# Kernel optimization log

Measured on AMD Instinct MI355X. Metric: run time of the kernel, lower is better.

Reference implementation:

```python
import jax, jax.numpy as jnp
import numpy as np

B, T = 64, 500
NUM_CONCEPT, DIM, SIZE_MEM = 1024, 64, 50


def setup_inputs() -> dict:
    key = jax.random.key(0)
    ks = jax.random.split(key, 16)
    d = DIM

    def lin(k, fin, fout):
        k1, k2 = jax.random.split(k)
        s = 1.0 / np.sqrt(fin)
        return (jax.random.uniform(k1, (fin, fout), jnp.float32, -s, s),
                jax.random.uniform(k2, (fout,), jnp.float32, -s, s))

    Wf, bf = lin(ks[4], 2 * d, d)
    We, be = lin(ks[5], d, d)
    Wa, ba = lin(ks[6], d, d)
    Wab, bab = lin(ks[7], d, 1)
    Wd, bd = lin(ks[8], d, 1)
    return {
        'concept_seq': jax.random.randint(ks[0], (B, T), 0, NUM_CONCEPT),
        'correct_seq': jax.random.randint(ks[1], (B, T), 0, 2),
        'num_concept': NUM_CONCEPT,
        'embed_key': jax.random.normal(ks[2], (NUM_CONCEPT, d), jnp.float32),
        'embed_value': jax.random.normal(ks[3], (2 * NUM_CONCEPT, d), jnp.float32),
        'Mk': jax.random.normal(ks[9], (SIZE_MEM, d), jnp.float32) * np.sqrt(2.0 / d),
        'Mv0': jax.random.normal(ks[10], (SIZE_MEM, d), jnp.float32) * np.sqrt(2.0 / d),
        'Wf': Wf, 'bf': bf, 'We': We, 'be': be, 'Wa': Wa, 'ba': ba,
        'Wab': Wab, 'bab': bab, 'Wd': Wd, 'bd': bd,
    }


def _forward(concept_seq, correct_seq, num_concept, embed_key, embed_value,
             Mk, Mv0, Wf, bf, We, be, Wa, ba, Wab, bab, Wd, bd):
    x = concept_seq + num_concept * correct_seq          # [B,T]
    k = embed_key[concept_seq]                           # [B,T,d]
    v = embed_value[x]                                   # [B,T,d]
    w = jax.nn.softmax(jnp.einsum('btd,sd->bts', k, Mk), axis=-1)  # [B,T,S]
    e = jax.nn.sigmoid(v @ We + be)                      # [B,T,d]
    a = jnp.tanh(v @ Wa + ba)                            # [B,T,d]

    bsz = concept_seq.shape[0]
    Mv_init = jnp.broadcast_to(Mv0, (bsz,) + Mv0.shape)  # [B,S,d]

    def step(Mvt, inp):
        wt, et, at = inp                                 # [B,S],[B,d],[B,d]
        u = wt[:, :, None]
        Mv_new = Mvt * (1.0 - u * et[:, None, :]) + u * at[:, None, :]
        return Mv_new, Mvt                               # emit pre-update state

    wT = jnp.swapaxes(w, 0, 1)                           # [T,B,S]
    eT = jnp.swapaxes(e, 0, 1)
    aT = jnp.swapaxes(a, 0, 1)
    _, Mv_pre = jax.lax.scan(step, Mv_init, (wT, eT, aT))  # [T,B,S,d]

    r = jnp.einsum('tbs,tbsd->btd', wT, Mv_pre)          # read content [B,T,d]
    f = jnp.tanh(jnp.concatenate([r, k], axis=-1) @ Wf + bf)
    stu_ability = jnp.tanh(f @ Wab + bab)                # [B,T,1] (dropout = eval identity)
    que_diff = jnp.tanh(k @ Wd + bd)                     # [B,T,1]
    return jax.nn.sigmoid(3.0 * stu_ability - que_diff)[..., 0]  # [B,T]


def reference(concept_seq, correct_seq, num_concept, embed_key, embed_value,
              Mk, Mv0, Wf, bf, We, be, Wa, ba, Wab, bab, Wd, bd):
    return _forward(concept_seq, correct_seq, num_concept, embed_key, embed_value,
                    Mk, Mv0, Wf, bf, We, be, Wa, ba, Wab, bab, Wd, bd)
```

## Files before the change

kernel.cpp:

```cpp
#include <hip/hip_runtime.h>
#include <hip/hip_bf16.h>
#include <math.h>

#define BB 64
#define TT 500
#define DD 64
#define SS 50
#define CH 20
#define NCH (TT / CH)

typedef float v2f __attribute__((ext_vector_type(2)));

__device__ __forceinline__ float sigmoidf_(float x) { return 1.0f / (1.0f + __expf(-x)); }

#define PIN() asm volatile("" ::: "memory")

__global__ __launch_bounds__(64) void k1_tables(
    const float* __restrict__ embed_key,
    const float* __restrict__ embed_value,
    const float* __restrict__ Mk,
    const float* __restrict__ We, const float* __restrict__ be,
    const float* __restrict__ Wa, const float* __restrict__ ba,
    int ncon, int nv,
    float* __restrict__ wTab, float* __restrict__ eaTab)
{
    const int lane = threadIdx.x;
    if ((int)blockIdx.x < ncon) {
        const int c = blockIdx.x;
        __shared__ float mkS[SS][DD + 1];
        __shared__ float kS[DD];
        kS[lane] = embed_key[c * DD + lane];
        for (int s = 0; s < SS; ++s)
            mkS[s][lane] = Mk[s * DD + lane];
        __syncthreads();

        float sc = -1e30f;
        if (lane < SS) {
            float acc = 0.f;
            #pragma unroll
            for (int dd = 0; dd < DD; ++dd)
                acc = fmaf(kS[dd], mkS[lane][dd], acc);
            sc = acc;
        }
        float m = sc;
        #pragma unroll
        for (int off = 32; off >= 1; off >>= 1)
            m = fmaxf(m, __shfl_xor(m, off));
        float ex = (lane < SS) ? __expf(sc - m) : 0.f;
        float ssum = ex;
        #pragma unroll
        for (int off = 32; off >= 1; off >>= 1)
            ssum += __shfl_xor(ssum, off);
        if (lane < SS)
            wTab[c * SS + lane] = ex / ssum;
    } else {
        const int x = blockIdx.x - ncon;
        __shared__ float vS[DD];
        vS[lane] = embed_value[x * DD + lane];
        __syncthreads();
        float acc_e = be[lane];
        float acc_a = ba[lane];
        #pragma unroll
        for (int i = 0; i < DD; ++i) {
            const float vi = vS[i];
            acc_e = fmaf(vi, We[i * DD + lane], acc_e);
            acc_a = fmaf(vi, Wa[i * DD + lane], acc_a);
        }
        float2 ea;
        ea.x = sigmoidf_(acc_e);
        ea.y = tanhf(acc_a);
        *(float2*)&eaTab[((size_t)x * DD + lane) * 2] = ea;
    }
}

#define STAGE_ISSUE(T0) {                                                    \
    _Pragma("unroll")                                                        \
    for (int kk = 0; kk < 5; ++kk) {                                         \
        const int idx_ = lane + 64 * kk;                                     \
        const int tt_ = idx_ >> 4, j_ = idx_ & 15;                           \
        const int s_ = st + j_;                                              \
        wr[kk] = (s_ < en) ? wTab[cL[(T0) + tt_] * SS + s_] : 0.f;           \
    }                                                                        \
    _Pragma("unroll")                                                        \
    for (int tt = 0; tt < CH; ++tt) {                                        \
        const int xx_ = xL[(T0) + tt];                                       \
        ear[tt] = *(const float2*)&eaTab[((size_t)xx_ * DD + lane) * 2];     \
    } }

#define STAGE_WRITE(BUF) {                                                   \
    _Pragma("unroll")                                                        \
    for (int kk = 0; kk < 5; ++kk) {                                         \
        const int idx_ = lane + 64 * kk;                                     \
        wL[BUF][idx_ >> 4][idx_ & 15] = wr[kk];                              \
    }                                                                        \
    _Pragma("unroll")                                                        \
    for (int tt = 0; tt < CH; ++tt)                                          \
        eaL[BUF][tt][lane] = ear[tt];                                        \
    }

#define PKSTEP(W2, JJ) {                                                     \
    const v2f mv_ = Mv2[JJ];                                                 \
    r2 = __builtin_elementwise_fma(W2, mv_, r2);                             \
    const v2f g_ = __builtin_elementwise_fma(e2, mv_, na2);                  \
    Mv2[JJ] = __builtin_elementwise_fma(-(W2), g_, mv_); }

__global__ __launch_bounds__(64, 1) void k2_scan(
    const int* __restrict__ cseq,
    const int* __restrict__ corr,
    const int* __restrict__ ncp,
    const float* __restrict__ wTab,
    const float* __restrict__ eaTab,
    const float* __restrict__ Mv0,
    float* __restrict__ rPart)
{
    const int b = blockIdx.x >> 2;
    const int sgB = blockIdx.x & 3;
    const int lane = threadIdx.x;
    const int nc = ncp[0];

    __shared__ int xL[TT];
    __shared__ int cL[TT];
    __shared__ float __align__(16) wL[2][CH][16];
    __shared__ float2 __align__(8) eaL[2][CH][DD];

    for (int i = lane; i < TT; i += 64) {
        const int c = cseq[b * TT + i];
        cL[i] = c;
        xL[i] = c + nc * corr[b * TT + i];
    }
    __syncthreads();

    const int st = (SS * sgB) >> 2;
    const int en = (SS * (sgB + 1)) >> 2;

    v2f Mv2[7];
    #pragma unroll
    for (int jj = 0; jj < 7; ++jj) {
        const int s0 = st + 2 * jj, s1 = s0 + 1;
        v2f m;
        m.x = (s0 < en) ? Mv0[s0 * DD + lane] : 0.f;
        m.y = (s1 < en) ? Mv0[s1 * DD + lane] : 0.f;
        Mv2[jj] = m;
    }

    float* rp = rPart + ((size_t)sgB * BB + b) * TT * DD + lane;

    float wr[5];
    float2 ear[CH];

    STAGE_ISSUE(0)
    STAGE_WRITE(0)

    for (int ch = 0; ch < NCH; ++ch) {
        const int buf = ch & 1;
        if (ch + 1 < NCH) {
            STAGE_ISSUE((ch + 1) * CH)
            PIN();
        }
        const int T0 = ch * CH;
        #pragma unroll
        for (int tc = 0; tc < CH; ++tc) {
            const float4 wq0 = *(const float4*)&wL[buf][tc][0];
            const float4 wq1 = *(const float4*)&wL[buf][tc][4];
            const float4 wq2 = *(const float4*)&wL[buf][tc][8];
            const v2f   w6_ = *(const v2f*)  &wL[buf][tc][12];
            const float2 ea = eaL[buf][tc][lane];
            const v2f e2  = {ea.x, ea.x};
            const v2f na2 = {-ea.y, -ea.y};
            const v2f w0_ = {wq0.x, wq0.y};
            const v2f w1_ = {wq0.z, wq0.w};
            const v2f w2_ = {wq1.x, wq1.y};
            const v2f w3_ = {wq1.z, wq1.w};
            const v2f w4_ = {wq2.x, wq2.y};
            const v2f w5_ = {wq2.z, wq2.w};
            v2f r2 = {0.f, 0.f};
            PKSTEP(w0_, 0) PKSTEP(w1_, 1) PKSTEP(w2_, 2) PKSTEP(w3_, 3)
            PKSTEP(w4_, 4) PKSTEP(w5_, 5) PKSTEP(w6_, 6)
            rp[(size_t)(T0 + tc) * DD] = r2.x + r2.y;
        }
        if (ch + 1 < NCH)
            STAGE_WRITE((ch + 1) & 1)
    }
}

__global__ __launch_bounds__(256) void k3_output(
    const int* __restrict__ cseq,
    const float* __restrict__ embed_key,
    const float* __restrict__ rPart,
    const float* __restrict__ Wf, const float* __restrict__ bf,
    const float* __restrict__ Wab, const float* __restrict__ bab,
    const float* __restrict__ Wd, const float* __restrict__ bd,
    float* __restrict__ out)
{
    const int tid = threadIdx.x;
    const int tx = tid & 15, ty = tid >> 4;
    const int bt0 = blockIdx.x * 64;

    __shared__ float __align__(16) wfS[128][64];
    __shared__ float __align__(16) catT[128][68];
    __shared__ float qS[64];
    __shared__ float wdS[64];
    __shared__ float redS[64][17];

    #pragma unroll
    for (int k = 0; k < 8; ++k) {
        const int idx = tid + k * 256;
        ((float4*)wfS)[idx] = ((const float4*)Wf)[idx];
    }
    if (tid < 64) wdS[tid] = Wd[tid];

    {
        const int d = tid & 63;
        const int g = tid >> 6;
        #pragma unroll
        for (int m = 0; m < 16; ++m) {
            const int btl = g + 4 * m;
            const int bt = bt0 + btl;
            const int c = cseq[bt];
            const size_t o = (size_t)bt * DD + d;
            const float r = rPart[o]
                          + rPart[(size_t)1 * BB * TT * DD + o]
                          + rPart[(size_t)2 * BB * TT * DD + o]
                          + rPart[(size_t)3 * BB * TT * DD + o];
            catT[d][btl] = r;
            catT[64 + d][btl] = embed_key[c * DD + d];
        }
    }
    __syncthreads();

    if (tid < 64) {
        const int btl = tid;
        float q = 0.f;
        #pragma unroll
        for (int i = 0; i < DD; ++i)
            q = fmaf(catT[64 + i][btl], wdS[i], q);
        qS[btl] = q;
    }

    float acc[4][4] = {{0.f}};
    #pragma unroll 8
    for (int i = 0; i < 128; ++i) {
        const float4 wf = *(const float4*)&wfS[i][tx * 4];
        const float4 ct = *(const float4*)&catT[i][ty * 4];
        acc[0][0] = fmaf(ct.x, wf.x, acc[0][0]);
        acc[0][1] = fmaf(ct.x, wf.y, acc[0][1]);
        acc[0][2] = fmaf(ct.x, wf.z, acc[0][2]);
        acc[0][3] = fmaf(ct.x, wf.w, acc[0][3]);
        acc[1][0] = fmaf(ct.y, wf.x, acc[1][0]);
        acc[1][1] = fmaf(ct.y, wf.y, acc[1][1]);
        acc[1][2] = fmaf(ct.y, wf.z, acc[1][2]);
        acc[1][3] = fmaf(ct.y, wf.w, acc[1][3]);
        acc[2][0] = fmaf(ct.z, wf.x, acc[2][0]);
        acc[2][1] = fmaf(ct.z, wf.y, acc[2][1]);
        acc[2][2] = fmaf(ct.z, wf.z, acc[2][2]);
        acc[2][3] = fmaf(ct.z, wf.w, acc[2][3]);
        acc[3][0] = fmaf(ct.w, wf.x, acc[3][0]);
        acc[3][1] = fmaf(ct.w, wf.y, acc[3][1]);
        acc[3][2] = fmaf(ct.w, wf.z, acc[3][2]);
        acc[3][3] = fmaf(ct.w, wf.w, acc[3][3]);
    }

    #pragma unroll
    for (int ii = 0; ii < 4; ++ii) {
        float p = 0.f;
        #pragma unroll
        for (int jj = 0; jj < 4; ++jj) {
            const int j = tx * 4 + jj;
            const float f = tanhf(acc[ii][jj] + bf[j]);
            p = fmaf(f, Wab[j], p);
        }
        redS[ty * 4 + ii][tx] = p;
    }
    __syncthreads();

    if (tid < 64) {
        const int btl = tid;
        float s = 0.f;
        #pragma unroll
        for (int t2 = 0; t2 < 16; ++t2)
            s += redS[btl][t2];
        const float stu  = tanhf(s + bab[0]);
        const float diff = tanhf(qS[btl] + bd[0]);
        out[bt0 + btl] = sigmoidf_(3.0f * stu - diff);
    }
}

extern "C" void kernel_launch(void* const* d_in, const int* in_sizes, int n_in,
                              void* d_out, int out_size, void* d_ws, size_t ws_size,
                              hipStream_t stream)
{
    const int*   concept_seq = (const int*)  d_in[0];
    const int*   correct_seq = (const int*)  d_in[1];
    const int*   num_concept = (const int*)  d_in[2];
    const float* embed_key   = (const float*)d_in[3];
    const float* embed_value = (const float*)d_in[4];
    const float* Mk          = (const float*)d_in[5];
    const float* Mv0         = (const float*)d_in[6];
    const float* Wf          = (const float*)d_in[7];
    const float* bf          = (const float*)d_in[8];
    const float* We          = (const float*)d_in[9];
    const float* be          = (const float*)d_in[10];
    const float* Wa          = (const float*)d_in[11];
    const float* ba          = (const float*)d_in[12];
    const float* Wab         = (const float*)d_in[13];
    const float* bab         = (const float*)d_in[14];
    const float* Wd          = (const float*)d_in[15];
    const float* bd          = (const float*)d_in[16];
    float* out = (float*)d_out;

    const int NCON = in_sizes[3] / DD;
    const int NV   = in_sizes[4] / DD;

    float* wTab  = (float*)d_ws;
    float* eaTab = wTab + (size_t)NCON * SS;
    float* rPart = eaTab + (size_t)NV * DD * 2;

    k1_tables<<<NCON + NV, 64, 0, stream>>>(
        embed_key, embed_value, Mk, We, be, Wa, ba,
        NCON, NV, wTab, eaTab);

    k2_scan<<<BB * 4, 64, 0, stream>>>(
        concept_seq, correct_seq, num_concept,
        wTab, eaTab, Mv0, rPart);

    k3_output<<<(BB * TT) / 64, 256, 0, stream>>>(
        concept_seq, embed_key, rPart,
        Wf, bf, Wab, bab, Wd, bd, out);
}
```

Before: 170.7 us.

## Parallelize memory scan over time with chunked affine maps and replay

Replaces the sequential 500-step per-batch scan with a three-phase parallel scan. Each of 10 time chunks first computes its per-slot affine map (A, B). A combine kernel then chains those maps to get each chunk's starting memory state, and a replay kernel reruns every chunk from its start state to produce the read vectors. The four slot-group partial reads are also reduced in shared memory inside the replay kernel, so k3 reads a single r buffer instead of summing four partial buffers. This exposes far more blocks (640 vs 256) to the GPU at the cost of roughly doubling the scan arithmetic, adding two extra launches, and writing and reading extra A/B buffers.

```diff
diff --git a/kernel.cpp b/kernel.cpp
--- a/kernel.cpp
+++ b/kernel.cpp
@@ -6,14 +6,12 @@
 #define TT 500
 #define DD 64
 #define SS 50
-#define CH 20
-#define NCH (TT / CH)
+#define PP 10
+#define LL 50
 
 typedef float v2f __attribute__((ext_vector_type(2)));
 
 __device__ __forceinline__ float sigmoidf_(float x) { return 1.0f / (1.0f + __expf(-x)); }
-
-#define PIN() asm volatile("" ::: "memory")
 
 __global__ __launch_bounds__(64) void k1_tables(
     const float* __restrict__ embed_key,
@@ -73,120 +71,163 @@
     }
 }
 
-#define STAGE_ISSUE(T0) {                                                    \
-    _Pragma("unroll")                                                        \
-    for (int kk = 0; kk < 5; ++kk) {                                         \
-        const int idx_ = lane + 64 * kk;                                     \
-        const int tt_ = idx_ >> 4, j_ = idx_ & 15;                           \
-        const int s_ = st + j_;                                              \
-        wr[kk] = (s_ < en) ? wTab[cL[(T0) + tt_] * SS + s_] : 0.f;           \
-    }                                                                        \
-    _Pragma("unroll")                                                        \
-    for (int tt = 0; tt < CH; ++tt) {                                        \
-        const int xx_ = xL[(T0) + tt];                                       \
-        ear[tt] = *(const float2*)&eaTab[((size_t)xx_ * DD + lane) * 2];     \
-    } }
-
-#define STAGE_WRITE(BUF) {                                                   \
-    _Pragma("unroll")                                                        \
-    for (int kk = 0; kk < 5; ++kk) {                                         \
-        const int idx_ = lane + 64 * kk;                                     \
-        wL[BUF][idx_ >> 4][idx_ & 15] = wr[kk];                              \
-    }                                                                        \
-    _Pragma("unroll")                                                        \
-    for (int tt = 0; tt < CH; ++tt)                                          \
-        eaL[BUF][tt][lane] = ear[tt];                                        \
-    }
-
-#define PKSTEP(W2, JJ) {                                                     \
-    const v2f mv_ = Mv2[JJ];                                                 \
-    r2 = __builtin_elementwise_fma(W2, mv_, r2);                             \
-    const v2f g_ = __builtin_elementwise_fma(e2, mv_, na2);                  \
-    Mv2[JJ] = __builtin_elementwise_fma(-(W2), g_, mv_); }
-
-__global__ __launch_bounds__(64, 1) void k2_scan(
-    const int* __restrict__ cseq,
-    const int* __restrict__ corr,
+
+#define SCAN_STAGE()                                                          \
+    const int b = blockIdx.x / PP, p = blockIdx.x % PP;                       \
+    const int tid = threadIdx.x;                                              \
+    const int lane = tid & 63, sg = tid >> 6;                                 \
+    const int t0g = p * LL;                                                   \
+    if (tid < LL) {                                                           \
+        const int c = cseq[b * TT + t0g + tid];                               \
+        cL[tid] = c;                                                          \
+        xL[tid] = c + ncp[0] * corr[b * TT + t0g + tid];                      \
+    }                                                                         \
+    __syncthreads();                                                          \
+    for (int i = tid; i < LL * 64; i += 256) {                                \
+        const int t = i >> 6, l = i & 63;                                     \
+        const int sg_ = l >> 4, j_ = l & 15;                                  \
+        const int st_ = (SS * sg_) >> 2, en_ = (SS * (sg_ + 1)) >> 2;         \
+        const int s_ = st_ + j_;                                              \
+        wLds[t][l] = (s_ < en_) ? wTab[cL[t] * SS + s_] : 0.f;                \
+        eaLds[t][l] = *(const float2*)&eaTab[((size_t)xL[t] * DD + l) * 2];   \
+    }
+
+#define LOADW(t)                                                              \
+    const float4 wv0 = *(const float4*)&wLds[t][sg * 16];                     \
+    const float4 wv1 = *(const float4*)&wLds[t][sg * 16 + 4];                 \
+    const float4 wv2 = *(const float4*)&wLds[t][sg * 16 + 8];                 \
+    const v2f w6 = *(const v2f*)&wLds[t][sg * 16 + 12];                       \
+    const v2f w[7] = {{wv0.x, wv0.y}, {wv0.z, wv0.w}, {wv1.x, wv1.y},         \
+                      {wv1.z, wv1.w}, {wv2.x, wv2.y}, {wv2.z, wv2.w}, w6};
+
+__global__ __launch_bounds__(256) void k2a_maps(
+    const int* __restrict__ cseq, const int* __restrict__ corr,
     const int* __restrict__ ncp,
-    const float* __restrict__ wTab,
-    const float* __restrict__ eaTab,
+    const float* __restrict__ wTab, const float* __restrict__ eaTab,
+    float* __restrict__ Aout, float* __restrict__ Bout)
+{
+    __shared__ int cL[LL], xL[LL];
+    __shared__ float __align__(16) wLds[LL][64];
+    __shared__ float2 __align__(8) eaLds[LL][64];
+
+    SCAN_STAGE()
+    __syncthreads();
+
+    v2f A[7], Bc[7];
+    #pragma unroll
+    for (int j = 0; j < 7; ++j) { A[j] = (v2f){1.f, 1.f}; Bc[j] = (v2f){0.f, 0.f}; }
+
+    const v2f one2 = {1.f, 1.f};
+    #pragma unroll 2
+    for (int t = 0; t < LL; ++t) {
+        LOADW(t)
+        const float2 ea = eaLds[t][lane];
+        const v2f e2 = {ea.x, ea.x}, a2 = {ea.y, ea.y};
+        #pragma unroll
+        for (int j = 0; j < 7; ++j) {
+            const v2f al = __builtin_elementwise_fma(-w[j], e2, one2);
+            const v2f be = w[j] * a2;
+            A[j]  = al * A[j];
+            Bc[j] = __builtin_elementwise_fma(al, Bc[j], be);
+        }
+    }
+
+    const int st = (SS * sg) >> 2, en = (SS * (sg + 1)) >> 2;
+    float* Ap = Aout + (size_t)blockIdx.x * SS * DD;
+    float* Bp = Bout + (size_t)blockIdx.x * SS * DD;
+    #pragma unroll
+    for (int j = 0; j < 6; ++j) {
+        const int s0 = st + 2 * j;
+        Ap[(size_t)s0 * DD + lane] = A[j].x;
+        Ap[(size_t)(s0 + 1) * DD + lane] = A[j].y;
+        Bp[(size_t)s0 * DD + lane] = Bc[j].x;
+        Bp[(size_t)(s0 + 1) * DD + lane] = Bc[j].y;
+    }
+    if (st + 12 < en) {
+        Ap[(size_t)(st + 12) * DD + lane] = A[6].x;
+        Bp[(size_t)(st + 12) * DD + lane] = Bc[6].x;
+    }
+}
+
+__global__ __launch_bounds__(256) void k2b_combine(
     const float* __restrict__ Mv0,
-    float* __restrict__ rPart)
-{
-    const int b = blockIdx.x >> 2;
-    const int sgB = blockIdx.x & 3;
-    const int lane = threadIdx.x;
-    const int nc = ncp[0];
-
-    __shared__ int xL[TT];
-    __shared__ int cL[TT];
-    __shared__ float __align__(16) wL[2][CH][16];
-    __shared__ float2 __align__(8) eaL[2][CH][DD];
-
-    for (int i = lane; i < TT; i += 64) {
-        const int c = cseq[b * TT + i];
-        cL[i] = c;
-        xL[i] = c + nc * corr[b * TT + i];
+    float* __restrict__ Aio, const float* __restrict__ Bin)
+{
+    const int gid = blockIdx.x * 256 + threadIdx.x;
+    const int d = gid & 63;
+    const int s = (gid >> 6) % SS;
+    const int b = gid / (SS * 64);
+    float m = Mv0[s * DD + d];
+    #pragma unroll
+    for (int p = 0; p < PP; ++p) {
+        const size_t o = (((size_t)(b * PP + p)) * SS + s) * DD + d;
+        const float a = Aio[o], bb = Bin[o];
+        m = fmaf(a, m, bb);
+        Aio[o] = m;
+    }
+}
+
+__global__ __launch_bounds__(256) void k2c_replay(
+    const int* __restrict__ cseq, const int* __restrict__ corr,
+    const int* __restrict__ ncp,
+    const float* __restrict__ wTab, const float* __restrict__ eaTab,
+    const float* __restrict__ Mv0, const float* __restrict__ Mst,
+    float* __restrict__ rOut)
+{
+    __shared__ int cL[LL], xL[LL];
+    __shared__ float __align__(16) wLds[LL][64];
+    __shared__ float2 __align__(8) eaLds[LL][64];
+    __shared__ float parts[10][4][DD];
+
+    SCAN_STAGE()
+
+    const int st = (SS * sg) >> 2, en = (SS * (sg + 1)) >> 2;
+    const float* msrc = (p == 0) ? Mv0
+                       : (Mst + (size_t)(b * PP + p - 1) * SS * DD);
+    v2f m[7];
+    #pragma unroll
+    for (int j = 0; j < 7; ++j) {
+        const int s0 = st + 2 * j, s1 = s0 + 1;
+        v2f mm = {0.f, 0.f};
+        if (s0 < en) mm.x = msrc[(size_t)s0 * DD + lane];
+        if (s1 < en) mm.y = msrc[(size_t)s1 * DD + lane];
+        m[j] = mm;
     }
     __syncthreads();
 
-    const int st = (SS * sgB) >> 2;
-    const int en = (SS * (sgB + 1)) >> 2;
-
-    v2f Mv2[7];
-    #pragma unroll
-    for (int jj = 0; jj < 7; ++jj) {
-        const int s0 = st + 2 * jj, s1 = s0 + 1;
-        v2f m;
-        m.x = (s0 < en) ? Mv0[s0 * DD + lane] : 0.f;
-        m.y = (s1 < en) ? Mv0[s1 * DD + lane] : 0.f;
-        Mv2[jj] = m;
-    }
-
-    float* rp = rPart + ((size_t)sgB * BB + b) * TT * DD + lane;
-
-    float wr[5];
-    float2 ear[CH];
-
-    STAGE_ISSUE(0)
-    STAGE_WRITE(0)
-
-    for (int ch = 0; ch < NCH; ++ch) {
-        const int buf = ch & 1;
-        if (ch + 1 < NCH) {
-            STAGE_ISSUE((ch + 1) * CH)
-            PIN();
-        }
-        const int T0 = ch * CH;
-        #pragma unroll
-        for (int tc = 0; tc < CH; ++tc) {
-            const float4 wq0 = *(const float4*)&wL[buf][tc][0];
-            const float4 wq1 = *(const float4*)&wL[buf][tc][4];
-            const float4 wq2 = *(const float4*)&wL[buf][tc][8];
-            const v2f   w6_ = *(const v2f*)  &wL[buf][tc][12];
-            const float2 ea = eaL[buf][tc][lane];
-            const v2f e2  = {ea.x, ea.x};
-            const v2f na2 = {-ea.y, -ea.y};
-            const v2f w0_ = {wq0.x, wq0.y};
-            const v2f w1_ = {wq0.z, wq0.w};
-            const v2f w2_ = {wq1.x, wq1.y};
-            const v2f w3_ = {wq1.z, wq1.w};
-            const v2f w4_ = {wq2.x, wq2.y};
-            const v2f w5_ = {wq2.z, wq2.w};
+    float* rb = rOut + ((size_t)b * TT + p * LL) * DD;
+    for (int tq = 0; tq < LL / 10; ++tq) {
+        #pragma unroll
+        for (int u = 0; u < 10; ++u) {
+            const int t = tq * 10 + u;
+            LOADW(t)
+            const float2 ea = eaLds[t][lane];
+            const v2f e2 = {ea.x, ea.x}, na2 = {-ea.y, -ea.y};
             v2f r2 = {0.f, 0.f};
-            PKSTEP(w0_, 0) PKSTEP(w1_, 1) PKSTEP(w2_, 2) PKSTEP(w3_, 3)
-            PKSTEP(w4_, 4) PKSTEP(w5_, 5) PKSTEP(w6_, 6)
-            rp[(size_t)(T0 + tc) * DD] = r2.x + r2.y;
-        }
-        if (ch + 1 < NCH)
-            STAGE_WRITE((ch + 1) & 1)
+            #pragma unroll
+            for (int j = 0; j < 7; ++j) {
+                const v2f mv = m[j];
+                r2 = __builtin_elementwise_fma(w[j], mv, r2);
+                const v2f g = __builtin_elementwise_fma(e2, mv, na2);
+                m[j] = __builtin_elementwise_fma(-w[j], g, mv);
+            }
+            parts[u][sg][lane] = r2.x + r2.y;
+        }
+        __syncthreads();
+        for (int o = tid; o < 10 * DD; o += 256) {
+            const int u2 = o >> 6, d2 = o & 63;
+            rb[(size_t)(tq * 10 + u2) * DD + d2] =
+                parts[u2][0][d2] + parts[u2][1][d2]
+              + parts[u2][2][d2] + parts[u2][3][d2];
+        }
+        __syncthreads();
     }
 }
 
 __global__ __launch_bounds__(256) void k3_output(
     const int* __restrict__ cseq,
     const float* __restrict__ embed_key,
-    const float* __restrict__ rPart,
+    const float* __restrict__ rOut,
     const float* __restrict__ Wf, const float* __restrict__ bf,
     const float* __restrict__ Wab, const float* __restrict__ bab,
     const float* __restrict__ Wd, const float* __restrict__ bd,
@@ -213,16 +254,11 @@
         const int d = tid & 63;
         const int g = tid >> 6;
         #pragma unroll
-        for (int m = 0; m < 16; ++m) {
-            const int btl = g + 4 * m;
+        for (int mq = 0; mq < 16; ++mq) {
+            const int btl = g + 4 * mq;
             const int bt = bt0 + btl;
             const int c = cseq[bt];
-            const size_t o = (size_t)bt * DD + d;
-            const float r = rPart[o]
-                          + rPart[(size_t)1 * BB * TT * DD + o]
-                          + rPart[(size_t)2 * BB * TT * DD + o]
-                          + rPart[(size_t)3 * BB * TT * DD + o];
-            catT[d][btl] = r;
+            catT[d][btl] = rOut[(size_t)bt * DD + d];
             catT[64 + d][btl] = embed_key[c * DD + d];
         }
     }
@@ -262,14 +298,14 @@
 
     #pragma unroll
     for (int ii = 0; ii < 4; ++ii) {
-        float p = 0.f;
+        float pacc = 0.f;
         #pragma unroll
         for (int jj = 0; jj < 4; ++jj) {
             const int j = tx * 4 + jj;
             const float f = tanhf(acc[ii][jj] + bf[j]);
-            p = fmaf(f, Wab[j], p);
-        }
-        redS[ty * 4 + ii][tx] = p;
+            pacc = fmaf(f, Wab[j], pacc);
+        }
+        redS[ty * 4 + ii][tx] = pacc;
     }
     __syncthreads();
 
@@ -313,17 +349,26 @@
 
     float* wTab  = (float*)d_ws;
     float* eaTab = wTab + (size_t)NCON * SS;
-    float* rPart = eaTab + (size_t)NV * DD * 2;
+    float* Abuf  = eaTab + (size_t)NV * DD * 2;
+    float* Bbuf  = Abuf + (size_t)BB * PP * SS * DD;
+    float* rOut  = Bbuf + (size_t)BB * PP * SS * DD;
 
     k1_tables<<<NCON + NV, 64, 0, stream>>>(
         embed_key, embed_value, Mk, We, be, Wa, ba,
         NCON, NV, wTab, eaTab);
 
-    k2_scan<<<BB * 4, 64, 0, stream>>>(
+    k2a_maps<<<BB * PP, 256, 0, stream>>>(
         concept_seq, correct_seq, num_concept,
-        wTab, eaTab, Mv0, rPart);
+        wTab, eaTab, Abuf, Bbuf);
+
+    k2b_combine<<<(BB * SS * DD) / 256, 256, 0, stream>>>(
+        Mv0, Abuf, Bbuf);
+
+    k2c_replay<<<BB * PP, 256, 0, stream>>>(
+        concept_seq, correct_seq, num_concept,
+        wTab, eaTab, Mv0, Abuf, rOut);
 
     k3_output<<<(BB * TT) / 64, 256, 0, stream>>>(
-        concept_seq, embed_key, rPart,
+        concept_seq, embed_key, rOut,
         Wf, bf, Wab, bab, Wd, bd, out);
 }
```

New measurement: 152.6 us. 1.12x faster.
